# Performance work log

Hardware: AMD Instinct MI355X
Metric: run time of the kernel (lower is better)

Reference implementation:

```python
import jax, jax.numpy as jnp
import numpy as np

C_S = 1024
C_Z = 128
NUM_HEADS = 16
HEAD_DIM = C_S // NUM_HEADS
INF = 1000000.0
LN_EPS = 1e-5


def setup_inputs() -> dict:
    key = jax.random.key(0)
    ks = jax.random.split(key, 12)
    B, N = 2, 768
    s = jax.random.normal(ks[0], (B, N, C_S), dtype=jnp.float32)
    z = jax.random.normal(ks[1], (B, N, N, C_Z), dtype=jnp.float32)
    mask = jnp.ones((B, N), dtype=jnp.float32)
    k_in = jax.random.normal(ks[2], (B, N, C_S), dtype=jnp.float32)
    sc = 1.0 / np.sqrt(C_S)
    Wq = jax.random.normal(ks[3], (C_S, C_S), dtype=jnp.float32) * sc
    bq = jnp.zeros((C_S,), dtype=jnp.float32)
    Wk = jax.random.normal(ks[4], (C_S, C_S), dtype=jnp.float32) * sc
    Wv = jax.random.normal(ks[5], (C_S, C_S), dtype=jnp.float32) * sc
    Wg = jax.random.normal(ks[6], (C_S, C_S), dtype=jnp.float32) * sc
    ln_g = jnp.ones((C_Z,), dtype=jnp.float32)
    ln_b = jnp.zeros((C_Z,), dtype=jnp.float32)
    Wz = jax.random.normal(ks[7], (C_Z, NUM_HEADS), dtype=jnp.float32) / np.sqrt(C_Z)
    # NOTE: module zero-inits proj_o; use small random weights so output/grads are non-trivial.
    Wo = jax.random.normal(ks[8], (C_S, C_S), dtype=jnp.float32) * sc
    return {"s": s, "z": z, "mask": mask, "k_in": k_in,
            "Wq": Wq, "bq": bq, "Wk": Wk, "Wv": Wv, "Wg": Wg,
            "ln_g": ln_g, "ln_b": ln_b, "Wz": Wz, "Wo": Wo}


def reference(s, z, mask, k_in, Wq, bq, Wk, Wv, Wg, ln_g, ln_b, Wz, Wo):
    B, N, _ = s.shape
    H, D = NUM_HEADS, HEAD_DIM
    q = (s @ Wq + bq).reshape(B, N, H, D)
    k = (k_in @ Wk).reshape(B, N, H, D)
    v = (k_in @ Wv).reshape(B, N, H, D)
    # pair bias: LayerNorm(c_z) -> Linear(c_z -> H) -> (B, H, N, N)
    mu = z.mean(axis=-1, keepdims=True)
    var = ((z - mu) ** 2).mean(axis=-1, keepdims=True)
    zn = (z - mu) * jax.lax.rsqrt(var + LN_EPS) * ln_g + ln_b
    bias = jnp.transpose(zn @ Wz, (0, 3, 1, 2))  # (B, H, N, N)
    g = jax.nn.sigmoid(s @ Wg)  # (B, N, C_S)
    attn = jnp.einsum('bihd,bjhd->bhij', q, k) / np.sqrt(D) + bias
    attn = attn + (1.0 - mask)[:, None, None, :] * (-INF)
    p = jax.nn.softmax(attn, axis=-1)
    o = jnp.einsum('bhij,bjhd->bihd', p, v).reshape(B, N, C_S)
    return (g * o) @ Wo
```

## Files before the change

### kernel.cpp

```cpp
#include <hip/hip_runtime.h>
#include <cstdint>


#define B_  2
#define N_  768
#define CS_ 1024
#define CZ_ 128
#define NH_ 16
#define HD_ 64

typedef unsigned short bf16_t;
typedef __attribute__((ext_vector_type(4))) float f32x4;
typedef __attribute__((ext_vector_type(8))) short s16x8;

__device__ __forceinline__ float bflo(uint32_t u){ return __uint_as_float(u<<16); }
__device__ __forceinline__ float bfhi(uint32_t u){ return __uint_as_float(u & 0xFFFF0000u); }
__device__ __forceinline__ float bf2f(bf16_t u){ return __uint_as_float(((uint32_t)u)<<16); }
__device__ __forceinline__ bf16_t f2bf(float f){
  uint32_t x = __float_as_uint(f);
  return (bf16_t)((x + 0x7FFFu + ((x>>16)&1u)) >> 16);
}
__device__ __forceinline__ void unpack8(uint4 q, float* d){
  d[0]=bflo(q.x); d[1]=bfhi(q.x); d[2]=bflo(q.y); d[3]=bfhi(q.y);
  d[4]=bflo(q.z); d[5]=bfhi(q.z); d[6]=bflo(q.w); d[7]=bfhi(q.w);
}
__device__ __forceinline__ void load8f(const void* base, size_t idx, int isbf, float* d){
  if (isbf) { uint4 q = *(const uint4*)((const bf16_t*)base + idx); unpack8(q, d); }
  else {
    const float* p = (const float*)base + idx;
    float4 a = *(const float4*)p, b = *(const float4*)(p+4);
    d[0]=a.x; d[1]=a.y; d[2]=a.z; d[3]=a.w; d[4]=b.x; d[5]=b.y; d[6]=b.z; d[7]=b.w;
  }
}
__device__ __forceinline__ float load1f(const void* base, size_t idx, int isbf){
  return isbf ? bf2f(((const bf16_t*)base)[idx]) : ((const float*)base)[idx];
}
__device__ __forceinline__ void ld16bf(const void* base, size_t idx, int isbf, bf16_t* d){
  if (isbf) {
    const bf16_t* p = (const bf16_t*)base + idx;
    *(uint4*)d = *(const uint4*)p;
    *(uint4*)(d+8) = *(const uint4*)(p+8);
  } else {
    const float* p = (const float*)base + idx;
    #pragma unroll
    for (int e = 0; e < 16; ++e) d[e] = f2bf(p[e]);
  }
}

__global__ void detect_kernel(const uint32_t* __restrict__ mask_bits,
                              const void* __restrict__ Wz,
                              const void* __restrict__ ln_g,
                              const void* __restrict__ ln_b,
                              int* __restrict__ flag, float* __restrict__ AhCh)
{
  const int t = threadIdx.x;
  const int isbf = (mask_bits[0] == 0x3F803F80u) ? 1 : 0;
  if (t == 0) *flag = isbf;
  if (t < 16) {
    float a = 0.0f, c2 = 0.0f;
    for (int c = 0; c < CZ_; ++c) {
      const float w = load1f(Wz, (size_t)c*NH_ + t, isbf);
      a  += load1f(ln_g, c, isbf) * w;
      c2 += load1f(ln_b, c, isbf) * w;
    }
    AhCh[t] = a; AhCh[16 + t] = c2;
  }
}

__global__ __launch_bounds__(256) void prep_wt_kernel(
    const void* __restrict__ Wq, const void* __restrict__ Wk,
    const void* __restrict__ Wv, const void* __restrict__ Wg,
    const void* __restrict__ Wo, bf16_t* __restrict__ WT,
    const int* __restrict__ flagp)
{
  const int isbf = *flagp;
  const int w = blockIdx.z;
  const void* W = (w==0)?Wq:(w==1)?Wk:(w==2)?Wv:(w==3)?Wg:Wo;
  bf16_t* dst = WT + (size_t)w*CS_*CS_;
  __shared__ bf16_t T[64][72];
  const int t = threadIdx.x;
  const int r = t >> 2, c0 = (t & 3) * 16;
  const int k0 = blockIdx.x * 64, n0 = blockIdx.y * 64;
  __align__(16) bf16_t vv[16];
  ld16bf(W, (size_t)(k0 + r)*CS_ + n0 + c0, isbf, vv);
  #pragma unroll
  for (int e = 0; e < 16; ++e) T[r][c0 + e] = vv[e];
  __syncthreads();
  __align__(16) bf16_t ov[16];
  #pragma unroll
  for (int e = 0; e < 16; ++e) ov[e] = T[c0 + e][r];
  bf16_t* op = dst + (size_t)(n0 + r)*CS_ + k0 + c0;
  *(uint4*)op = *(uint4*)&ov[0];
  *(uint4*)(op + 8) = *(uint4*)&ov[8];
}

__global__ __launch_bounds__(256) void pair_bias_kernel(
    const void* __restrict__ z, const void* __restrict__ ln_g,
    const void* __restrict__ Wz, const float* __restrict__ AhCh,
    float* __restrict__ S, const int* __restrict__ flagp)
{
  const int isbf = *flagp;
  __shared__ float Wp[CZ_*NH_];
  const int t = threadIdx.x;
  {
    float wv[8];
    load8f(Wz, (size_t)t*8, isbf, wv);
    const float gc = load1f(ln_g, t >> 1, isbf);
    #pragma unroll
    for (int e = 0; e < 8; ++e) Wp[t*8 + e] = gc * wv[e];
  }
  __syncthreads();

  const int j = blockIdx.x*256 + t, i = blockIdx.y, b = blockIdx.z;
  const size_t zbase = (((size_t)(b*N_ + i))*N_ + j)*CZ_;

  float d[16] = {};
  float s1 = 0.0f, s2 = 0.0f;
  #pragma unroll 2
  for (int cc = 0; cc < CZ_; cc += 8) {
    float zv[8];
    load8f(z, zbase + cc, isbf, zv);
    #pragma unroll
    for (int e = 0; e < 8; ++e) {
      const float zz = zv[e];
      s1 += zz; s2 = fmaf(zz, zz, s2);
      const float4 w0 = *(const float4*)&Wp[(cc+e)*16 + 0];
      const float4 w1 = *(const float4*)&Wp[(cc+e)*16 + 4];
      const float4 w2 = *(const float4*)&Wp[(cc+e)*16 + 8];
      const float4 w3 = *(const float4*)&Wp[(cc+e)*16 + 12];
      d[ 0] = fmaf(zz, w0.x, d[ 0]); d[ 1] = fmaf(zz, w0.y, d[ 1]);
      d[ 2] = fmaf(zz, w0.z, d[ 2]); d[ 3] = fmaf(zz, w0.w, d[ 3]);
      d[ 4] = fmaf(zz, w1.x, d[ 4]); d[ 5] = fmaf(zz, w1.y, d[ 5]);
      d[ 6] = fmaf(zz, w1.z, d[ 6]); d[ 7] = fmaf(zz, w1.w, d[ 7]);
      d[ 8] = fmaf(zz, w2.x, d[ 8]); d[ 9] = fmaf(zz, w2.y, d[ 9]);
      d[10] = fmaf(zz, w2.z, d[10]); d[11] = fmaf(zz, w2.w, d[11]);
      d[12] = fmaf(zz, w3.x, d[12]); d[13] = fmaf(zz, w3.y, d[13]);
      d[14] = fmaf(zz, w3.z, d[14]); d[15] = fmaf(zz, w3.w, d[15]);
    }
  }
  const float mu  = s1 * (1.0f/CZ_);
  const float var = s2 * (1.0f/CZ_) - mu*mu;
  const float rs  = rsqrtf(var + 1e-5f);
  const float am  = -rs * mu;

  float Ah[16], Ch[16];
  #pragma unroll
  for (int p = 0; p < 4; ++p) {
    *(float4*)&Ah[p*4] = *(const float4*)&AhCh[p*4];
    *(float4*)&Ch[p*4] = *(const float4*)&AhCh[16 + p*4];
  }
  const size_t sbase = ((size_t)b*NH_*N_ + i)*N_ + j;
  #pragma unroll
  for (int h = 0; h < 16; ++h) {
    const float bias = fmaf(rs, d[h], fmaf(am, Ah[h], Ch[h]));
    S[sbase + (size_t)h*N_*N_] = bias;
  }
}

__global__ __launch_bounds__(256) void qkvg_mfma_kernel(
    const void* __restrict__ s_in, const void* __restrict__ kin,
    const bf16_t* __restrict__ WT, const void* __restrict__ bq,
    bf16_t* __restrict__ q, bf16_t* __restrict__ k,
    bf16_t* __restrict__ v, float* __restrict__ g,
    const int* __restrict__ flagp)
{
  const int isbf = *flagp;
  __shared__ bf16_t As[128*40];
  __shared__ bf16_t Bs[128*40];
  const int t = threadIdx.x;
  const int bn = blockIdx.x, bm = blockIdx.y;
  const int proj = bn >> 3;
  const void* A = (proj == 0 || proj == 3) ? s_in : kin;
  const bf16_t* WTp = WT + (size_t)proj*CS_*CS_;
  const int n0 = (bn & 7) * 128, m0 = bm * 128;
  const int lane = t & 63, wid = t >> 6;
  const int wr = wid >> 1, wc = wid & 1;
  const int l16 = lane & 15, lq = lane >> 4;
  const int srow = t >> 1, scol = (t & 1) * 16;
  f32x4 acc[4][4] = {};

  for (int k0 = 0; k0 < CS_; k0 += 32) {
    __align__(16) bf16_t av[16];
    ld16bf(A, (size_t)(m0 + srow)*CS_ + k0 + scol, isbf, av);
    {
      const bf16_t* bp = WTp + (size_t)(n0 + srow)*CS_ + k0 + scol;
      *(uint4*)&Bs[srow*40 + scol]     = *(const uint4*)bp;
      *(uint4*)&Bs[srow*40 + scol + 8] = *(const uint4*)(bp + 8);
    }
    *(uint4*)&As[srow*40 + scol]     = *(uint4*)&av[0];
    *(uint4*)&As[srow*40 + scol + 8] = *(uint4*)&av[8];
    __syncthreads();
    s16x8 af[4], bfg[4];
    #pragma unroll
    for (int m = 0; m < 4; ++m)
      af[m] = *(const s16x8*)&As[(wr*64 + m*16 + l16)*40 + lq*8];
    #pragma unroll
    for (int n = 0; n < 4; ++n)
      bfg[n] = *(const s16x8*)&Bs[(wc*64 + n*16 + l16)*40 + lq*8];
    #pragma unroll
    for (int m = 0; m < 4; ++m)
      #pragma unroll
      for (int n = 0; n < 4; ++n)
        acc[m][n] = __builtin_amdgcn_mfma_f32_16x16x32_bf16(af[m], bfg[n], acc[m][n], 0, 0, 0);
    __syncthreads();
  }

  #pragma unroll
  for (int n = 0; n < 4; ++n) {
    const int gc = n0 + wc*64 + n*16 + l16;
    float bqv = 0.0f;
    if (proj == 0) bqv = load1f(bq, gc, isbf);
    #pragma unroll
    for (int m = 0; m < 4; ++m) {
      #pragma unroll
      for (int r = 0; r < 4; ++r) {
        const int gr = m0 + wr*64 + m*16 + lq*4 + r;
        const float val = acc[m][n][r];
        const size_t off = (size_t)gr*CS_ + gc;
        if      (proj == 0) q[off] = f2bf(val + bqv);
        else if (proj == 1) k[off] = f2bf(val);
        else if (proj == 2) v[off] = f2bf(val);
        else                g[off] = 1.0f/(1.0f + __expf(-val));
      }
    }
  }
}

__global__ __launch_bounds__(256) void vt_kernel(
    const bf16_t* __restrict__ v, bf16_t* __restrict__ vt)
{
  __shared__ bf16_t T[64][72];
  const int t = threadIdx.x;
  const int jt = blockIdx.x, bh = blockIdx.y, b = bh >> 4, h = bh & 15;
  const int r = t >> 2, c0 = (t & 3) * 16;
  const int j0 = jt * 64;
  const bf16_t* vp = v + ((size_t)(b*N_ + j0 + r))*CS_ + h*HD_ + c0;
  *(uint4*)&T[r][c0]     = *(const uint4*)vp;
  *(uint4*)&T[r][c0 + 8] = *(const uint4*)(vp + 8);
  __syncthreads();
  __align__(16) bf16_t ov[16];
  #pragma unroll
  for (int e = 0; e < 16; ++e) ov[e] = T[c0 + e][r];
  bf16_t* op = vt + ((size_t)bh*HD_ + r)*N_ + j0 + c0;
  *(uint4*)op       = *(uint4*)&ov[0];
  *(uint4*)(op + 8) = *(uint4*)&ov[8];
}

#define KPITCH 76
#define VPITCH 136
__global__ __launch_bounds__(256) void flash_kernel(
    const bf16_t* __restrict__ q, const bf16_t* __restrict__ k,
    const bf16_t* __restrict__ vt, const float* __restrict__ biasS,
    const void* __restrict__ mask, const float* __restrict__ g,
    bf16_t* __restrict__ go, const int* __restrict__ flagp)
{
  const int isbf = *flagp;
  __shared__ bf16_t Qs[64*72];
  __shared__ bf16_t Ks[128*KPITCH];
  __shared__ bf16_t Vs[64*VPITCH];
  __shared__ bf16_t Ps[64*VPITCH];
  const int t = threadIdx.x;
  const int mi = blockIdx.x, bh = blockIdx.y, b = bh >> 4, h = bh & 15;
  const int lane = t & 63, wid = t >> 6;
  const int l16 = lane & 15, lq = lane >> 4;
  const int i0 = mi * 64;
  const int wrow = wid * 16;

  {
    const int r = t >> 2, c0 = (t & 3) * 16;
    const bf16_t* qp = q + ((size_t)(b*N_ + i0 + r))*CS_ + h*HD_ + c0;
    *(uint4*)&Qs[r*72 + c0]     = *(const uint4*)qp;
    *(uint4*)&Qs[r*72 + c0 + 8] = *(const uint4*)(qp + 8);
  }

  float m_st[4], l_st[4];
  #pragma unroll
  for (int r = 0; r < 4; ++r) { m_st[r] = -1.0e30f; l_st[r] = 0.0f; }
  f32x4 oacc[4] = {};

  for (int j0 = 0; j0 < N_; j0 += 128) {
    {
      const int r = t >> 1, c0 = (t & 1) * 32;
      const bf16_t* kp = k + ((size_t)(b*N_ + j0 + r))*CS_ + h*HD_ + c0;
      #pragma unroll
      for (int e = 0; e < 4; ++e)
        *(uint4*)&Ks[r*KPITCH + c0 + e*8] = *(const uint4*)(kp + e*8);
      const int vr = t >> 2, vc = (t & 3) * 32;
      const bf16_t* vp = vt + ((size_t)bh*HD_ + vr)*N_ + j0 + vc;
      #pragma unroll
      for (int e = 0; e < 4; ++e)
        *(uint4*)&Vs[vr*VPITCH + vc + e*8] = *(const uint4*)(vp + e*8);
    }
    __syncthreads();

    f32x4 sacc[8] = {};
    #pragma unroll
    for (int kc = 0; kc < 2; ++kc) {
      const s16x8 af = *(const s16x8*)&Qs[(wrow + l16)*72 + kc*32 + lq*8];
      s16x8 bfg[8];
      #pragma unroll
      for (int n = 0; n < 8; ++n)
        bfg[n] = *(const s16x8*)&Ks[(n*16 + l16)*KPITCH + kc*32 + lq*8];
      #pragma unroll
      for (int n = 0; n < 8; ++n)
        sacc[n] = __builtin_amdgcn_mfma_f32_16x16x32_bf16(af, bfg[n], sacc[n], 0, 0, 0);
    }

    float madd[8];
    #pragma unroll
    for (int n = 0; n < 8; ++n) {
      const int gj = j0 + n*16 + l16;
      madd[n] = (1.0f - load1f(mask, (size_t)b*N_ + gj, isbf)) * (-1.0e6f);
    }
    float pvv[8][4];
    float scl[4];
    #pragma unroll
    for (int r = 0; r < 4; ++r) {
      const int gi = i0 + wrow + lq*4 + r;
      const float* bp = biasS + ((size_t)bh*N_ + gi)*N_ + j0;
      float tmax = -1.0e30f;
      #pragma unroll
      for (int n = 0; n < 8; ++n) {
        const float sv = fmaf(sacc[n][r], 0.125f, bp[n*16 + l16]) + madd[n];
        pvv[n][r] = sv;
        tmax = fmaxf(tmax, sv);
      }
      #pragma unroll
      for (int msk = 1; msk <= 8; msk <<= 1)
        tmax = fmaxf(tmax, __shfl_xor(tmax, msk));
      const float newm = fmaxf(m_st[r], tmax);
      scl[r] = __expf(m_st[r] - newm);
      float rsum = 0.0f;
      #pragma unroll
      for (int n = 0; n < 8; ++n) {
        const float p = __expf(pvv[n][r] - newm);
        pvv[n][r] = p;
        rsum += p;
      }
      #pragma unroll
      for (int msk = 1; msk <= 8; msk <<= 1)
        rsum += __shfl_xor(rsum, msk);
      l_st[r] = l_st[r] * scl[r] + rsum;
      m_st[r] = newm;
    }
    #pragma unroll
    for (int n = 0; n < 4; ++n)
      #pragma unroll
      for (int r = 0; r < 4; ++r)
        oacc[n][r] *= scl[r];

    #pragma unroll
    for (int n = 0; n < 8; ++n)
      #pragma unroll
      for (int r = 0; r < 4; ++r)
        Ps[(wrow + lq*4 + r)*VPITCH + n*16 + l16] = f2bf(pvv[n][r]);
    __syncthreads();

    #pragma unroll
    for (int kc = 0; kc < 4; ++kc) {
      const s16x8 af = *(const s16x8*)&Ps[(wrow + l16)*VPITCH + kc*32 + lq*8];
      s16x8 bfg[4];
      #pragma unroll
      for (int n = 0; n < 4; ++n)
        bfg[n] = *(const s16x8*)&Vs[(n*16 + l16)*VPITCH + kc*32 + lq*8];
      #pragma unroll
      for (int n = 0; n < 4; ++n)
        oacc[n] = __builtin_amdgcn_mfma_f32_16x16x32_bf16(af, bfg[n], oacc[n], 0, 0, 0);
    }
    __syncthreads();
  }

  #pragma unroll
  for (int r = 0; r < 4; ++r) {
    const float rl = 1.0f / l_st[r];
    const int gi = i0 + wrow + lq*4 + r;
    #pragma unroll
    for (int n = 0; n < 4; ++n) {
      const int gd = h*HD_ + n*16 + l16;
      const size_t off = ((size_t)(b*N_ + gi))*CS_ + gd;
      const float val = oacc[n][r] * rl;
      go[off] = f2bf(g[off] * val);
    }
  }
}

__global__ __launch_bounds__(256) void final_mfma_kernel(
    const bf16_t* __restrict__ go, const bf16_t* __restrict__ WoT,
    void* __restrict__ out, const int* __restrict__ flagp)
{
  const int isbf = *flagp;
  __shared__ bf16_t As[64*40];
  __shared__ bf16_t Bs[64*40];
  const int t = threadIdx.x;
  const int n0 = blockIdx.x * 64, m0 = blockIdx.y * 64;
  const int lane = t & 63, wid = t >> 6;
  const int wr = wid >> 1, wc = wid & 1;
  const int l16 = lane & 15, lq = lane >> 4;
  const int srow = t >> 2, scol = (t & 3) * 8;
  f32x4 acc[2][2] = {};

  for (int k0 = 0; k0 < CS_; k0 += 32) {
    *(uint4*)&As[srow*40 + scol] = *(const uint4*)(go  + (size_t)(m0 + srow)*CS_ + k0 + scol);
    *(uint4*)&Bs[srow*40 + scol] = *(const uint4*)(WoT + (size_t)(n0 + srow)*CS_ + k0 + scol);
    __syncthreads();
    s16x8 af[2], bfg[2];
    #pragma unroll
    for (int m = 0; m < 2; ++m)
      af[m] = *(const s16x8*)&As[(wr*32 + m*16 + l16)*40 + lq*8];
    #pragma unroll
    for (int n = 0; n < 2; ++n)
      bfg[n] = *(const s16x8*)&Bs[(wc*32 + n*16 + l16)*40 + lq*8];
    #pragma unroll
    for (int m = 0; m < 2; ++m)
      #pragma unroll
      for (int n = 0; n < 2; ++n)
        acc[m][n] = __builtin_amdgcn_mfma_f32_16x16x32_bf16(af[m], bfg[n], acc[m][n], 0, 0, 0);
    __syncthreads();
  }
  #pragma unroll
  for (int m = 0; m < 2; ++m)
    #pragma unroll
    for (int n = 0; n < 2; ++n)
      #pragma unroll
      for (int r = 0; r < 4; ++r) {
        const int gm = m0 + wr*32 + m*16 + lq*4 + r;
        const int gn = n0 + wc*32 + n*16 + l16;
        const float val = acc[m][n][r];
        if (isbf) ((bf16_t*)out)[(size_t)gm*CS_ + gn] = f2bf(val);
        else      ((float*)out)[(size_t)gm*CS_ + gn] = val;
      }
}

extern "C" void kernel_launch(void* const* d_in, const int* in_sizes, int n_in,
                              void* d_out, int out_size, void* d_ws, size_t ws_size,
                              hipStream_t stream)
{
  const void* s_in = d_in[0];
  const void* z    = d_in[1];
  const void* mask = d_in[2];
  const void* k_in = d_in[3];
  const void* Wq   = d_in[4];
  const void* bq   = d_in[5];
  const void* Wk   = d_in[6];
  const void* Wv   = d_in[7];
  const void* Wg   = d_in[8];
  const void* ln_g = d_in[9];
  const void* ln_b = d_in[10];
  const void* Wz   = d_in[11];
  const void* Wo   = d_in[12];

  int*   flag = (int*)d_ws;
  float* AhCh = (float*)d_ws + 16;
  char*  base = (char*)d_ws + 256;

  bf16_t* WT = (bf16_t*)(base);
  bf16_t* q  = (bf16_t*)(base + 10485760);
  bf16_t* k  = (bf16_t*)(base + 13631488);
  bf16_t* v  = (bf16_t*)(base + 16777216);
  bf16_t* vt = (bf16_t*)(base + 19922944);
  bf16_t* go = (bf16_t*)(base + 23068672);
  float*  g  = (float* )(base + 26214400);
  float*  S  = (float* )(base + 32505856);
  bf16_t* WoT = WT + (size_t)4*CS_*CS_;

  detect_kernel<<<1, 64, 0, stream>>>((const uint32_t*)mask, Wz, ln_g, ln_b, flag, AhCh);
  prep_wt_kernel<<<dim3(16, 16, 5), 256, 0, stream>>>(Wq, Wk, Wv, Wg, Wo, WT, flag);
  pair_bias_kernel<<<dim3(3, 768, 2), 256, 0, stream>>>(z, ln_g, Wz, AhCh, S, flag);
  qkvg_mfma_kernel<<<dim3(32, 12), 256, 0, stream>>>(s_in, k_in, WT, bq, q, k, v, g, flag);
  vt_kernel<<<dim3(12, 32), 256, 0, stream>>>(v, vt);
  flash_kernel<<<dim3(12, 32), 256, 0, stream>>>(q, k, vt, S, mask, g, go, flag);
  final_mfma_kernel<<<dim3(16, 24), 256, 0, stream>>>(go, WoT, d_out, flag);
}
```

Baseline: 1.014 ms.

## Use MFMA for pair bias, fuse V transpose into projection, share K/P LDS

The pair-bias kernel now stages a 128-row z tile in LDS as bf16, computes the LayerNorm statistics per row, and does the c_z→heads projection with bf16 MFMA instead of scalar FMAs. It also writes S with float4 stores along j. The QKVG projection writes V directly in transposed per-head layout, which removes the separate vt kernel and the intermediate v buffer. The flash kernel reuses the K LDS buffer for P, at the cost of one extra barrier per tile, to cut LDS use. Rounding z to bf16 before the projection adds precision risk.

```diff
diff --git a/kernel.cpp b/kernel.cpp
--- a/kernel.cpp
+++ b/kernel.cpp
@@ -94,66 +94,90 @@
   *(uint4*)(op + 8) = *(uint4*)&ov[8];
 }
 
-__global__ __launch_bounds__(256) void pair_bias_kernel(
+__global__ __launch_bounds__(256) void pair_bias_mfma_kernel(
     const void* __restrict__ z, const void* __restrict__ ln_g,
     const void* __restrict__ Wz, const float* __restrict__ AhCh,
     float* __restrict__ S, const int* __restrict__ flagp)
 {
   const int isbf = *flagp;
-  __shared__ float Wp[CZ_*NH_];
-  const int t = threadIdx.x;
+  __shared__ bf16_t Zs[128*136];
+  __shared__ bf16_t Wps[16*136];
+  __shared__ float  RsAm[128*2];
+  const int t = threadIdx.x;
+  const int jb = blockIdx.x, i = blockIdx.y, b = blockIdx.z;
+  const int j0 = jb * 128;
+  const int lane = t & 63, wid = t >> 6;
+  const int l16 = lane & 15, lq = lane >> 4;
+
+  if (t < 128) {
+    float wv[16];
+    load8f(Wz, (size_t)t*NH_,     isbf, wv);
+    load8f(Wz, (size_t)t*NH_ + 8, isbf, wv + 8);
+    const float gc = load1f(ln_g, t, isbf);
+    #pragma unroll
+    for (int h = 0; h < 16; ++h) Wps[h*136 + t] = f2bf(gc * wv[h]);
+  }
+
+  const size_t ztile = (((size_t)(b*N_ + i))*N_ + j0) * CZ_;
+  #pragma unroll
+  for (int it = 0; it < 8; ++it) {
+    const int e0 = it*2048 + t*8;
+    const int rr = e0 >> 7, cc = e0 & 127;
+    __align__(16) bf16_t tmp[8];
+    if (isbf) {
+      *(uint4*)tmp = *(const uint4*)((const bf16_t*)z + ztile + e0);
+    } else {
+      const float* p = (const float*)z + ztile + e0;
+      float4 a = *(const float4*)p, b4 = *(const float4*)(p + 4);
+      tmp[0]=f2bf(a.x);  tmp[1]=f2bf(a.y);  tmp[2]=f2bf(a.z);  tmp[3]=f2bf(a.w);
+      tmp[4]=f2bf(b4.x); tmp[5]=f2bf(b4.y); tmp[6]=f2bf(b4.z); tmp[7]=f2bf(b4.w);
+    }
+    *(uint4*)&Zs[rr*136 + cc] = *(uint4*)tmp;
+  }
+  __syncthreads();
+
   {
-    float wv[8];
-    load8f(Wz, (size_t)t*8, isbf, wv);
-    const float gc = load1f(ln_g, t >> 1, isbf);
-    #pragma unroll
-    for (int e = 0; e < 8; ++e) Wp[t*8 + e] = gc * wv[e];
+    const int r = t >> 1, hc = t & 1;
+    float s1 = 0.0f, s2 = 0.0f;
+    #pragma unroll
+    for (int e = 0; e < 8; ++e) {
+      uint4 qv = *(const uint4*)&Zs[r*136 + hc*64 + e*8];
+      float d8[8]; unpack8(qv, d8);
+      #pragma unroll
+      for (int x = 0; x < 8; ++x) { s1 += d8[x]; s2 = fmaf(d8[x], d8[x], s2); }
+    }
+    const float c1 = s1 + __shfl_xor(s1, 1);
+    const float c2 = s2 + __shfl_xor(s2, 1);
+    if (hc == 0) {
+      const float mu  = c1 * (1.0f/CZ_);
+      const float var = c2 * (1.0f/CZ_) - mu*mu;
+      const float rs  = rsqrtf(var + 1e-5f);
+      RsAm[r*2]   = rs;
+      RsAm[r*2+1] = -rs * mu;
+    }
   }
   __syncthreads();
 
-  const int j = blockIdx.x*256 + t, i = blockIdx.y, b = blockIdx.z;
-  const size_t zbase = (((size_t)(b*N_ + i))*N_ + j)*CZ_;
-
-  float d[16] = {};
-  float s1 = 0.0f, s2 = 0.0f;
-  #pragma unroll 2
-  for (int cc = 0; cc < CZ_; cc += 8) {
-    float zv[8];
-    load8f(z, zbase + cc, isbf, zv);
-    #pragma unroll
-    for (int e = 0; e < 8; ++e) {
-      const float zz = zv[e];
-      s1 += zz; s2 = fmaf(zz, zz, s2);
-      const float4 w0 = *(const float4*)&Wp[(cc+e)*16 + 0];
-      const float4 w1 = *(const float4*)&Wp[(cc+e)*16 + 4];
-      const float4 w2 = *(const float4*)&Wp[(cc+e)*16 + 8];
-      const float4 w3 = *(const float4*)&Wp[(cc+e)*16 + 12];
-      d[ 0] = fmaf(zz, w0.x, d[ 0]); d[ 1] = fmaf(zz, w0.y, d[ 1]);
-      d[ 2] = fmaf(zz, w0.z, d[ 2]); d[ 3] = fmaf(zz, w0.w, d[ 3]);
-      d[ 4] = fmaf(zz, w1.x, d[ 4]); d[ 5] = fmaf(zz, w1.y, d[ 5]);
-      d[ 6] = fmaf(zz, w1.z, d[ 6]); d[ 7] = fmaf(zz, w1.w, d[ 7]);
-      d[ 8] = fmaf(zz, w2.x, d[ 8]); d[ 9] = fmaf(zz, w2.y, d[ 9]);
-      d[10] = fmaf(zz, w2.z, d[10]); d[11] = fmaf(zz, w2.w, d[11]);
-      d[12] = fmaf(zz, w3.x, d[12]); d[13] = fmaf(zz, w3.y, d[13]);
-      d[14] = fmaf(zz, w3.z, d[14]); d[15] = fmaf(zz, w3.w, d[15]);
-    }
-  }
-  const float mu  = s1 * (1.0f/CZ_);
-  const float var = s2 * (1.0f/CZ_) - mu*mu;
-  const float rs  = rsqrtf(var + 1e-5f);
-  const float am  = -rs * mu;
-
-  float Ah[16], Ch[16];
-  #pragma unroll
-  for (int p = 0; p < 4; ++p) {
-    *(float4*)&Ah[p*4] = *(const float4*)&AhCh[p*4];
-    *(float4*)&Ch[p*4] = *(const float4*)&AhCh[16 + p*4];
-  }
-  const size_t sbase = ((size_t)b*NH_*N_ + i)*N_ + j;
-  #pragma unroll
-  for (int h = 0; h < 16; ++h) {
-    const float bias = fmaf(rs, d[h], fmaf(am, Ah[h], Ch[h]));
-    S[sbase + (size_t)h*N_*N_] = bias;
+  const float Ahv = AhCh[l16], Chv = AhCh[16 + l16];
+  #pragma unroll
+  for (int gg = 0; gg < 2; ++gg) {
+    const int row0 = wid*32 + gg*16;
+    f32x4 acc = {};
+    #pragma unroll
+    for (int kc = 0; kc < 4; ++kc) {
+      const s16x8 af  = *(const s16x8*)&Zs[(row0 + l16)*136 + kc*32 + lq*8];
+      const s16x8 bfg = *(const s16x8*)&Wps[l16*136 + kc*32 + lq*8];
+      acc = __builtin_amdgcn_mfma_f32_16x16x32_bf16(af, bfg, acc, 0, 0, 0);
+    }
+    const int lbase = row0 + lq*4;
+    float o4[4];
+    #pragma unroll
+    for (int rr = 0; rr < 4; ++rr) {
+      const float rs = RsAm[(lbase+rr)*2], am = RsAm[(lbase+rr)*2+1];
+      o4[rr] = fmaf(rs, acc[rr], fmaf(am, Ahv, Chv));
+    }
+    float* Sp = S + (((size_t)(b*NH_ + l16))*N_ + i)*N_ + j0 + lbase;
+    *(float4*)Sp = make_float4(o4[0], o4[1], o4[2], o4[3]);
   }
 }
 
@@ -161,7 +185,7 @@
     const void* __restrict__ s_in, const void* __restrict__ kin,
     const bf16_t* __restrict__ WT, const void* __restrict__ bq,
     bf16_t* __restrict__ q, bf16_t* __restrict__ k,
-    bf16_t* __restrict__ v, float* __restrict__ g,
+    bf16_t* __restrict__ vt, float* __restrict__ g,
     const int* __restrict__ flagp)
 {
   const int isbf = *flagp;
@@ -205,45 +229,41 @@
     __syncthreads();
   }
 
-  #pragma unroll
-  for (int n = 0; n < 4; ++n) {
-    const int gc = n0 + wc*64 + n*16 + l16;
-    float bqv = 0.0f;
-    if (proj == 0) bqv = load1f(bq, gc, isbf);
-    #pragma unroll
-    for (int m = 0; m < 4; ++m) {
-      #pragma unroll
-      for (int r = 0; r < 4; ++r) {
-        const int gr = m0 + wr*64 + m*16 + lq*4 + r;
-        const float val = acc[m][n][r];
-        const size_t off = (size_t)gr*CS_ + gc;
-        if      (proj == 0) q[off] = f2bf(val + bqv);
-        else if (proj == 1) k[off] = f2bf(val);
-        else if (proj == 2) v[off] = f2bf(val);
-        else                g[off] = 1.0f/(1.0f + __expf(-val));
+  if (proj == 2) {
+    const int bb = bm / 6;
+    #pragma unroll
+    for (int n = 0; n < 4; ++n) {
+      const int gc = n0 + wc*64 + n*16 + l16;
+      const int h = gc >> 6, d = gc & 63;
+      #pragma unroll
+      for (int m = 0; m < 4; ++m) {
+        const int tok0 = m0 - bb*N_ + wr*64 + m*16 + lq*4;
+        ushort4 u;
+        u.x = f2bf(acc[m][n][0]); u.y = f2bf(acc[m][n][1]);
+        u.z = f2bf(acc[m][n][2]); u.w = f2bf(acc[m][n][3]);
+        *(ushort4*)(vt + (((size_t)(bb*NH_ + h))*HD_ + d)*N_ + tok0) = u;
       }
     }
-  }
-}
-
-__global__ __launch_bounds__(256) void vt_kernel(
-    const bf16_t* __restrict__ v, bf16_t* __restrict__ vt)
-{
-  __shared__ bf16_t T[64][72];
-  const int t = threadIdx.x;
-  const int jt = blockIdx.x, bh = blockIdx.y, b = bh >> 4, h = bh & 15;
-  const int r = t >> 2, c0 = (t & 3) * 16;
-  const int j0 = jt * 64;
-  const bf16_t* vp = v + ((size_t)(b*N_ + j0 + r))*CS_ + h*HD_ + c0;
-  *(uint4*)&T[r][c0]     = *(const uint4*)vp;
-  *(uint4*)&T[r][c0 + 8] = *(const uint4*)(vp + 8);
-  __syncthreads();
-  __align__(16) bf16_t ov[16];
-  #pragma unroll
-  for (int e = 0; e < 16; ++e) ov[e] = T[c0 + e][r];
-  bf16_t* op = vt + ((size_t)bh*HD_ + r)*N_ + j0 + c0;
-  *(uint4*)op       = *(uint4*)&ov[0];
-  *(uint4*)(op + 8) = *(uint4*)&ov[8];
+  } else {
+    #pragma unroll
+    for (int n = 0; n < 4; ++n) {
+      const int gc = n0 + wc*64 + n*16 + l16;
+      float bqv = 0.0f;
+      if (proj == 0) bqv = load1f(bq, gc, isbf);
+      #pragma unroll
+      for (int m = 0; m < 4; ++m) {
+        #pragma unroll
+        for (int r = 0; r < 4; ++r) {
+          const int gr = m0 + wr*64 + m*16 + lq*4 + r;
+          const float val = acc[m][n][r];
+          const size_t off = (size_t)gr*CS_ + gc;
+          if      (proj == 0) q[off] = f2bf(val + bqv);
+          else if (proj == 1) k[off] = f2bf(val);
+          else                g[off] = 1.0f/(1.0f + __expf(-val));
+        }
+      }
+    }
+  }
 }
 
 #define KPITCH 76
@@ -256,9 +276,8 @@
 {
   const int isbf = *flagp;
   __shared__ bf16_t Qs[64*72];
-  __shared__ bf16_t Ks[128*KPITCH];
+  __shared__ bf16_t KPs[128*KPITCH];
   __shared__ bf16_t Vs[64*VPITCH];
-  __shared__ bf16_t Ps[64*VPITCH];
   const int t = threadIdx.x;
   const int mi = blockIdx.x, bh = blockIdx.y, b = bh >> 4, h = bh & 15;
   const int lane = t & 63, wid = t >> 6;
@@ -284,7 +303,7 @@
       const bf16_t* kp = k + ((size_t)(b*N_ + j0 + r))*CS_ + h*HD_ + c0;
       #pragma unroll
       for (int e = 0; e < 4; ++e)
-        *(uint4*)&Ks[r*KPITCH + c0 + e*8] = *(const uint4*)(kp + e*8);
+        *(uint4*)&KPs[r*KPITCH + c0 + e*8] = *(const uint4*)(kp + e*8);
       const int vr = t >> 2, vc = (t & 3) * 32;
       const bf16_t* vp = vt + ((size_t)bh*HD_ + vr)*N_ + j0 + vc;
       #pragma unroll
@@ -300,11 +319,12 @@
       s16x8 bfg[8];
       #pragma unroll
       for (int n = 0; n < 8; ++n)
-        bfg[n] = *(const s16x8*)&Ks[(n*16 + l16)*KPITCH + kc*32 + lq*8];
+        bfg[n] = *(const s16x8*)&KPs[(n*16 + l16)*KPITCH + kc*32 + lq*8];
       #pragma unroll
       for (int n = 0; n < 8; ++n)
         sacc[n] = __builtin_amdgcn_mfma_f32_16x16x32_bf16(af, bfg[n], sacc[n], 0, 0, 0);
     }
+    __syncthreads();
 
     float madd[8];
     #pragma unroll
@@ -353,12 +373,12 @@
     for (int n = 0; n < 8; ++n)
       #pragma unroll
       for (int r = 0; r < 4; ++r)
-        Ps[(wrow + lq*4 + r)*VPITCH + n*16 + l16] = f2bf(pvv[n][r]);
+        KPs[(wrow + lq*4 + r)*VPITCH + n*16 + l16] = f2bf(pvv[n][r]);
     __syncthreads();
 
     #pragma unroll
     for (int kc = 0; kc < 4; ++kc) {
-      const s16x8 af = *(const s16x8*)&Ps[(wrow + l16)*VPITCH + kc*32 + lq*8];
+      const s16x8 af = *(const s16x8*)&KPs[(wrow + l16)*VPITCH + kc*32 + lq*8];
       s16x8 bfg[4];
       #pragma unroll
       for (int n = 0; n < 4; ++n)
@@ -456,18 +476,16 @@
   bf16_t* WT = (bf16_t*)(base);
   bf16_t* q  = (bf16_t*)(base + 10485760);
   bf16_t* k  = (bf16_t*)(base + 13631488);
-  bf16_t* v  = (bf16_t*)(base + 16777216);
-  bf16_t* vt = (bf16_t*)(base + 19922944);
-  bf16_t* go = (bf16_t*)(base + 23068672);
-  float*  g  = (float* )(base + 26214400);
-  float*  S  = (float* )(base + 32505856);
+  bf16_t* vt = (bf16_t*)(base + 16777216);
+  bf16_t* go = (bf16_t*)(base + 19922944);
+  float*  g  = (float* )(base + 23068672);
+  float*  S  = (float* )(base + 29360128);
   bf16_t* WoT = WT + (size_t)4*CS_*CS_;
 
   detect_kernel<<<1, 64, 0, stream>>>((const uint32_t*)mask, Wz, ln_g, ln_b, flag, AhCh);
   prep_wt_kernel<<<dim3(16, 16, 5), 256, 0, stream>>>(Wq, Wk, Wv, Wg, Wo, WT, flag);
-  pair_bias_kernel<<<dim3(3, 768, 2), 256, 0, stream>>>(z, ln_g, Wz, AhCh, S, flag);
-  qkvg_mfma_kernel<<<dim3(32, 12), 256, 0, stream>>>(s_in, k_in, WT, bq, q, k, v, g, flag);
-  vt_kernel<<<dim3(12, 32), 256, 0, stream>>>(v, vt);
+  pair_bias_mfma_kernel<<<dim3(6, 768, 2), 256, 0, stream>>>(z, ln_g, Wz, AhCh, S, flag);
+  qkvg_mfma_kernel<<<dim3(32, 12), 256, 0, stream>>>(s_in, k_in, WT, bq, q, k, vt, g, flag);
   flash_kernel<<<dim3(12, 32), 256, 0, stream>>>(q, k, vt, S, mask, g, go, flag);
   final_mfma_kernel<<<dim3(16, 24), 256, 0, stream>>>(go, WoT, d_out, flag);
 }
```

Result: faster. 963.5 us (-5.0%).
